# Kernel optimization log

Hardware: AMD Instinct MI355X
Metric: run time of the kernel (lower is better)

Reference implementation:

```python
import jax, jax.numpy as jnp
import numpy as np

N = 50000        # nodes
E = 800000       # directed edges (before self-loops)
NODE_DIM = 128
HIDDEN = 64
HEADS = 4
C = HIDDEN // HEADS   # 16 per-head channels
LAYERS = 4
G = 256          # graphs in batch
EPS = 1e-5       # BatchNorm eps
SLOPE = 0.2      # GAT leaky_relu negative slope


def setup_inputs() -> dict:
    key = jax.random.key(0)
    ks = jax.random.split(key, 12)

    def gl(k, shape, fan_in):  # glorot-ish init
        return jax.random.normal(k, shape, jnp.float32) * np.float32(1.0 / np.sqrt(fan_in))

    x = jax.random.normal(ks[0], (N, NODE_DIM), jnp.float32)
    edge_index = jax.random.randint(ks[1], (2, E), 0, N)
    batch = jnp.sort(jax.random.randint(ks[2], (N,), 0, G))

    return {
        "x": x,
        "embed_W": gl(ks[3], (NODE_DIM, HIDDEN), NODE_DIM),
        "embed_b": jnp.zeros((HIDDEN,), jnp.float32),
        "gat_W": gl(ks[4], (LAYERS, HIDDEN, HIDDEN), HIDDEN),
        "att_src": gl(ks[5], (LAYERS, HEADS, C), C),
        "att_dst": gl(ks[6], (LAYERS, HEADS, C), C),
        "gat_b": jnp.zeros((LAYERS, HIDDEN), jnp.float32),
        "bn_gamma": jnp.ones((LAYERS, HIDDEN), jnp.float32),
        "bn_beta": jnp.zeros((LAYERS, HIDDEN), jnp.float32),
        "fc1_W": gl(ks[7], (HIDDEN, HIDDEN), HIDDEN),
        "fc1_b": jnp.zeros((HIDDEN,), jnp.float32),
        "fc2_W": gl(ks[8], (HIDDEN, 1), HIDDEN),
        "fc2_b": jnp.zeros((1,), jnp.float32),
        "edge_index": edge_index,
        "batch": batch,
    }


def reference(x, embed_W, embed_b, gat_W, att_src, att_dst, gat_b,
              bn_gamma, bn_beta, fc1_W, fc1_b, fc2_W, fc2_b,
              edge_index, batch):
    # GATConv default: add self-loops (message flows src -> dst)
    loops = jnp.arange(N)
    src = jnp.concatenate([edge_index[0], loops])
    dst = jnp.concatenate([edge_index[1], loops])

    h = x @ embed_W + embed_b  # [N, HIDDEN]
    for l in range(LAYERS):
        xp = (h @ gat_W[l]).reshape(N, HEADS, C)          # per-head transform
        a_s = jnp.sum(xp * att_src[l], axis=-1)           # [N, H]
        a_d = jnp.sum(xp * att_dst[l], axis=-1)           # [N, H]
        e = jax.nn.leaky_relu(a_s[src] + a_d[dst], SLOPE) # [E', H]
        # segment softmax over incoming edges of each dst node
        m = jax.ops.segment_max(e, dst, num_segments=N)
        p = jnp.exp(e - m[dst])
        s = jax.ops.segment_sum(p, dst, num_segments=N)
        alpha = p / (s[dst] + 1e-16)                      # [E', H]
        msg = xp[src] * alpha[:, :, None]                 # [E', H, C]
        h = jax.ops.segment_sum(msg, dst, num_segments=N).reshape(N, HIDDEN) + gat_b[l]
        # BatchNorm over nodes (training-mode batch stats, biased variance)
        mu = jnp.mean(h, axis=0)
        var = jnp.var(h, axis=0)
        h = (h - mu) * jax.lax.rsqrt(var + EPS) * bn_gamma[l] + bn_beta[l]
        h = jax.nn.elu(h)

    g = jax.ops.segment_sum(h, batch, num_segments=G)     # global_add_pool
    g = jax.nn.relu(g @ fc1_W + fc1_b)                    # dropout: identity (eval)
    return (g @ fc2_W + fc2_b).reshape(-1)                # [G]
```

## Files before the change

kernel.cpp:

```cpp
#include <hip/hip_runtime.h>

#define N_NODES 50000
#define N_EDGES 800000
#define NODE_DIM 128
#define HIDDEN 64
#define HEADS 4
#define LAYERS 4
#define NGRAPH 256
#define BN_EPS 1e-5f
#define SLOPE 0.2f
#define NTILES 196
#define BN_BLOCKS 256
#define NPW 16
#define GBLK ((N_NODES + 4 * NPW - 1) / (4 * NPW))

typedef unsigned short u16;
typedef unsigned int   u32;

__device__ __forceinline__ float b2f(u16 v) { return __uint_as_float(((u32)v) << 16); }
__device__ __forceinline__ u16 f2b(float f) {
    u32 u = __float_as_uint(f);
    u32 r = (u + 0x7FFFu + ((u >> 16) & 1u)) >> 16;
    return (u16)r;
}
__device__ __forceinline__ float ld(const void* p, int i, int isf) {
    return isf ? ((const float*)p)[i] : b2f(((const u16*)p)[i]);
}

__global__ void k_mark(u16* out, u16 pat) { out[threadIdx.x] = pat; }

__global__ void k_initw(const void* gamma, const void* We, const void* b,
                        const void* gatW, int* flag, int* cnt,
                        float* __restrict__ Wf, float* __restrict__ bf) {
    int isf = (((const u32*)gamma)[0] == 0x3F800000u) ? 1 : 0;
    if (blockIdx.x < NTILES) {
        int i = blockIdx.x * 256 + threadIdx.x;
        if (i < N_NODES) cnt[i] = 0;
        if (i == 0) *flag = isf;
    } else {
        int r = blockIdx.x - NTILES;
        int c = threadIdx.x;
        if (c < HIDDEN) {
            float acc = 0.f;
            if (r < NODE_DIM) {
                for (int k = 0; k < HIDDEN; k++)
                    acc += ld(We, r * HIDDEN + k, isf) * ld(gatW, k * HIDDEN + c, isf);
                Wf[r * HIDDEN + c] = acc;
            } else {
                for (int k = 0; k < HIDDEN; k++)
                    acc += ld(b, k, isf) * ld(gatW, k * HIDDEN + c, isf);
                bf[c] = acc;
            }
        }
    }
}

__global__ void k_count(const int* __restrict__ ei, int* __restrict__ cnt,
                        int* __restrict__ eslot) {
    int e = blockIdx.x * 256 + threadIdx.x;
    if (e >= N_EDGES) return;
    eslot[e] = atomicAdd(&cnt[ei[N_EDGES + e]], 1);
}
__global__ void k_scan1(const int* __restrict__ cnt, int* __restrict__ row_ptr,
                        int* __restrict__ tsum) {
    int b = blockIdx.x, t = threadIdx.x, i = b * 256 + t;
    int c = (i < N_NODES) ? cnt[i] : 0;
    __shared__ int ps[256];
    ps[t] = c;
    __syncthreads();
    for (int off = 1; off < 256; off <<= 1) {
        int v = (t >= off) ? ps[t - off] : 0;
        __syncthreads();
        ps[t] += v;
        __syncthreads();
    }
    if (i < N_NODES) row_ptr[i] = ps[t] - c;
    if (t == 255) tsum[b] = ps[255];
}
__global__ void k_scan3(int* __restrict__ row_ptr, const int* __restrict__ tsum) {
    __shared__ int ps[256];
    int t = threadIdx.x;
    int c = (t < NTILES) ? tsum[t] : 0;
    ps[t] = c;
    __syncthreads();
    for (int off = 1; off < 256; off <<= 1) {
        int v = (t >= off) ? ps[t - off] : 0;
        __syncthreads();
        ps[t] += v;
        __syncthreads();
    }
    int toff_b = (blockIdx.x == 0) ? 0 : ps[blockIdx.x - 1];
    int i = blockIdx.x * 256 + t;
    if (i < N_NODES) row_ptr[i] += toff_b;
    if (i == 0) row_ptr[N_NODES] = N_EDGES;
}
__global__ void k_fill(const int* __restrict__ ei, const int* __restrict__ row_ptr,
                       const int* __restrict__ eslot, int* __restrict__ col) {
    int e = blockIdx.x * 256 + threadIdx.x;
    if (e >= N_EDGES) return;
    col[row_ptr[ei[N_EDGES + e]] + eslot[e]] = ei[e];
}

template<int ISF>
__device__ __forceinline__ float2 ldx2(const void* x, int n, int t) {
    if (ISF) {
        return ((const float2*)x)[(size_t)n * (NODE_DIM / 2) + t];
    } else {
        u32 v = ((const u32*)x)[(size_t)n * (NODE_DIM / 2) + t];
        return make_float2(__uint_as_float(v << 16), __uint_as_float(v & 0xFFFF0000u));
    }
}

template<int ISF>
__device__ __forceinline__ void xform0_body(const void* __restrict__ x,
                                            const float* __restrict__ Wf,
                                            const float* __restrict__ bf,
                                            const void* __restrict__ asrc,
                                            const void* __restrict__ adst,
                                            u16* __restrict__ xp16,
                                            float* __restrict__ a_s,
                                            float* __restrict__ a_d) {
    int w = threadIdx.x >> 6, t = threadIdx.x & 63;
    int n0 = blockIdx.x * (4 * NPW) + w * NPW;
    if (n0 >= N_NODES) return;
    __shared__ float xs[4][2][4][NODE_DIM];
    float wreg[NODE_DIM];
#pragma unroll
    for (int k = 0; k < NODE_DIM; k++) wreg[k] = Wf[k * HIDDEN + t];
    float bias = bf[t];
    float vsc = ld(asrc, t, ISF);
    float vdc = ld(adst, t, ISF);

    float2 r[4], rn[4];
#pragma unroll
    for (int i = 0; i < 4; i++) r[i] = ldx2<ISF>(x, n0 + i, t);
#pragma unroll
    for (int i = 0; i < 4; i++) *(float2*)&xs[w][0][i][2 * t] = r[i];

    for (int g = 0; g < NPW / 4; g++) {
        if (g + 1 < NPW / 4) {
#pragma unroll
            for (int i = 0; i < 4; i++) rn[i] = ldx2<ISF>(x, n0 + (g + 1) * 4 + i, t);
        }
#pragma unroll
        for (int i = 0; i < 4; i++) {
            int n = n0 + g * 4 + i;
            const float* xr = xs[w][g & 1][i];
            float a0 = 0.f, a1 = 0.f, a2 = 0.f, a3 = 0.f;
#pragma unroll
            for (int k = 0; k < NODE_DIM; k += 4) {
                float4 xv = *(const float4*)&xr[k];
                a0 += xv.x * wreg[k];
                a1 += xv.y * wreg[k + 1];
                a2 += xv.z * wreg[k + 2];
                a3 += xv.w * wreg[k + 3];
            }
            float acc = (a0 + a1) + (a2 + a3) + bias;
            xp16[(size_t)n * HIDDEN + t] = f2b(acc);
            float vs = acc * vsc, vd = acc * vdc;
#pragma unroll
            for (int o = 1; o < 16; o <<= 1) {
                vs += __shfl_xor(vs, o, 16);
                vd += __shfl_xor(vd, o, 16);
            }
            if ((t & 15) == 0) {
                a_s[n * HEADS + (t >> 4)] = vs;
                a_d[n * HEADS + (t >> 4)] = vd;
            }
        }
        if (g + 1 < NPW / 4) {
#pragma unroll
            for (int i = 0; i < 4; i++) *(float2*)&xs[w][(g + 1) & 1][i][2 * t] = rn[i];
        }
    }
}
__global__ void __launch_bounds__(256)
k_xform0(const void* __restrict__ x, const float* __restrict__ Wf,
         const float* __restrict__ bf,
         const void* __restrict__ asrc, const void* __restrict__ adst,
         const int* __restrict__ fl,
         u16* __restrict__ xp16, float* __restrict__ a_s, float* __restrict__ a_d,
         float* __restrict__ bn_part) {
    if (blockIdx.x < BN_BLOCKS && threadIdx.x < 128)
        bn_part[blockIdx.x * 128 + threadIdx.x] = 0.f;
    if (*fl) xform0_body<1>(x, Wf, bf, asrc, adst, xp16, a_s, a_d);
    else     xform0_body<0>(x, Wf, bf, asrc, adst, xp16, a_s, a_d);
}

template<int ISF>
__device__ __forceinline__ void transform_body(const float* __restrict__ h,
                                               const void* __restrict__ W,
                                               const void* __restrict__ asrc,
                                               const void* __restrict__ adst, int l,
                                               const float* __restrict__ bnss,
                                               u16* __restrict__ xp16,
                                               float* __restrict__ a_s,
                                               float* __restrict__ a_d) {
    int w = threadIdx.x >> 6, t = threadIdx.x & 63;
    int n0 = blockIdx.x * (4 * NPW) + w * NPW;
    if (n0 >= N_NODES) return;
    __shared__ float hsb[4][2][4][HIDDEN];
    float wreg[HIDDEN];
#pragma unroll
    for (int k = 0; k < HIDDEN; k++) wreg[k] = ld(W, l * HIDDEN * HIDDEN + k * HIDDEN + t, ISF);
    float vsc = ld(asrc, l * HIDDEN + t, ISF);
    float vdc = ld(adst, l * HIDDEN + t, ISF);
    float sc = bnss[t], sh = bnss[64 + t];

    float r[4], rn[4];
#pragma unroll
    for (int i = 0; i < 4; i++) {
        float u = h[(size_t)(n0 + i) * HIDDEN + t];
        u = u * sc + sh;
        r[i] = u > 0.f ? u : (__expf(u) - 1.f);
    }
#pragma unroll
    for (int i = 0; i < 4; i++) hsb[w][0][i][t] = r[i];

    for (int g = 0; g < NPW / 4; g++) {
        if (g + 1 < NPW / 4) {
#pragma unroll
            for (int i = 0; i < 4; i++)
                rn[i] = h[(size_t)(n0 + (g + 1) * 4 + i) * HIDDEN + t];
        }
#pragma unroll
        for (int i = 0; i < 4; i++) {
            int n = n0 + g * 4 + i;
            const float* hr = hsb[w][g & 1][i];
            float c0 = 0.f, c1 = 0.f, c2 = 0.f, c3 = 0.f;
#pragma unroll
            for (int k = 0; k < HIDDEN; k += 4) {
                float4 xv = *(const float4*)&hr[k];
                c0 += xv.x * wreg[k];
                c1 += xv.y * wreg[k + 1];
                c2 += xv.z * wreg[k + 2];
                c3 += xv.w * wreg[k + 3];
            }
            float acc = (c0 + c1) + (c2 + c3);
            xp16[(size_t)n * HIDDEN + t] = f2b(acc);
            float vs = acc * vsc, vd = acc * vdc;
#pragma unroll
            for (int o = 1; o < 16; o <<= 1) {
                vs += __shfl_xor(vs, o, 16);
                vd += __shfl_xor(vd, o, 16);
            }
            if ((t & 15) == 0) {
                a_s[n * HEADS + (t >> 4)] = vs;
                a_d[n * HEADS + (t >> 4)] = vd;
            }
        }
        if (g + 1 < NPW / 4) {
#pragma unroll
            for (int i = 0; i < 4; i++) {
                float u = rn[i] * sc + sh;
                hsb[w][(g + 1) & 1][i][t] = u > 0.f ? u : (__expf(u) - 1.f);
            }
        }
    }
}
__global__ void __launch_bounds__(256)
k_transform(const float* __restrict__ h, const void* __restrict__ W,
            const void* __restrict__ asrc, const void* __restrict__ adst,
            const int* __restrict__ fl, int l,
            const float* __restrict__ bnss,
            u16* __restrict__ xp16, float* __restrict__ a_s,
            float* __restrict__ a_d, float* __restrict__ bn_part) {
    if (blockIdx.x < BN_BLOCKS && threadIdx.x < 128)
        bn_part[blockIdx.x * 128 + threadIdx.x] = 0.f;
    if (*fl) transform_body<1>(h, W, asrc, adst, l, bnss, xp16, a_s, a_d);
    else     transform_body<0>(h, W, asrc, adst, l, bnss, xp16, a_s, a_d);
}

__global__ void __launch_bounds__(256)
k_gather(const int* __restrict__ row_ptr, const int* __restrict__ col,
         const float* __restrict__ a_s, const float* __restrict__ a_d,
         const u16* __restrict__ xp16, float* __restrict__ h,
         float* __restrict__ bn_part) {
    int d = blockIdx.x * 4 + (threadIdx.x >> 6);
    int t = threadIdx.x & 63;
    int hd = t >> 4, l16 = t & 15, hb = hd << 4;
    int beg = row_ptr[d], end = row_ptr[d + 1];
    float ad = a_d[d * HEADS + hd];

    float m = a_s[d * HEADS + hd] + ad;
    m = m > 0.f ? m : SLOPE * m;
    float s = 1.f;
    float acc = b2f(xp16[(size_t)d * HIDDEN + t]);

    for (int j0 = beg; j0 < end; j0 += 16) {
        int jj = j0 + l16;
        int sv = col[jj < end ? jj : end - 1];
        float e = -1e30f;
        if (jj < end) {
            e = a_s[sv * HEADS + hd] + ad;
            e = e > 0.f ? e : SLOPE * e;
        }
        float cm = e;
#pragma unroll
        for (int o = 1; o < 16; o <<= 1) cm = fmaxf(cm, __shfl_xor(cm, o, 16));
        float nm = fmaxf(m, cm);
        float scale = __expf(m - nm);
        float alpha = (jj < end) ? __expf(e - nm) : 0.f;
        float cs = alpha;
#pragma unroll
        for (int o = 1; o < 16; o <<= 1) cs += __shfl_xor(cs, o, 16);
        s = s * scale + cs;
        acc *= scale;
#pragma unroll
        for (int q = 0; q < 16; q++) {
            int   svq = __shfl(sv, q, 64);
            float aq  = __shfl(alpha, hb + q, 64);
            acc += aq * b2f(xp16[(size_t)svq * HIDDEN + t]);
        }
        m = nm;
    }
    float v = acc / (s + 1e-16f);
    h[(size_t)d * HIDDEN + t] = v;

    __shared__ float s1[256];
    __shared__ float s2[256];
    s1[threadIdx.x] = v;
    s2[threadIdx.x] = v * v;
    __syncthreads();
    if (threadIdx.x < 64) {
        float su = s1[t] + s1[64 + t] + s1[128 + t] + s1[192 + t];
        float sq = s2[t] + s2[64 + t] + s2[128 + t] + s2[192 + t];
        float* bp = bn_part + (blockIdx.x & (BN_BLOCKS - 1)) * 128;
        atomicAdd(bp + t, su);
        atomicAdd(bp + 64 + t, sq);
    }
}

__global__ void k_bn_final(const float* __restrict__ bn_part,
                           const void* __restrict__ gamma, const void* __restrict__ beta,
                           const int* __restrict__ fl, int l, float* __restrict__ bnss) {
    int t = threadIdx.x;
    float sum = 0.f, sq = 0.f;
#pragma unroll 8
    for (int b = 0; b < BN_BLOCKS; b++) {
        sum += bn_part[b * 128 + t];
        sq  += bn_part[b * 128 + 64 + t];
    }
    int isf = *fl;
    const float inv_n = 1.f / (float)N_NODES;
    float mu  = sum * inv_n;
    float var = sq * inv_n - mu * mu;
    float sc = rsqrtf(var + BN_EPS) * ld(gamma, l * HIDDEN + t, isf);
    bnss[t]      = sc;
    bnss[64 + t] = ld(beta, l * HIDDEN + t, isf) - mu * sc;
}

__global__ void __launch_bounds__(1024)
k_poolmlp(const float* __restrict__ h, const int* __restrict__ batch,
          const float* __restrict__ bnss,
          const void* __restrict__ W1, const void* __restrict__ b1,
          const void* __restrict__ W2, const void* __restrict__ b2,
          const int* __restrict__ fl, void* __restrict__ out) {
    int gr = blockIdx.x;
    int t = threadIdx.x & 63, w = threadIdx.x >> 6;
    int lo = 0, hi = N_NODES;
    while (lo < hi) { int mid = (lo + hi) >> 1; if (batch[mid] < gr) lo = mid + 1; else hi = mid; }
    int beg = lo;
    lo = 0; hi = N_NODES;
    while (lo < hi) { int mid = (lo + hi) >> 1; if (batch[mid] < gr + 1) lo = mid + 1; else hi = mid; }
    int end = lo;
    float sc = bnss[t], sh = bnss[64 + t];
    float acc = 0.f;
    for (int n = beg + w; n < end; n += 16) {
        float v = h[(size_t)n * HIDDEN + t] * sc + sh;
        acc += v > 0.f ? v : (__expf(v) - 1.f);
    }
    __shared__ float sd[1024];
    __shared__ float gs[64];
    sd[threadIdx.x] = acc;
    __syncthreads();
    if (w < 8) sd[threadIdx.x] += sd[threadIdx.x + 512];
    __syncthreads();
    if (w < 4) sd[threadIdx.x] += sd[threadIdx.x + 256];
    __syncthreads();
    if (w < 2) sd[threadIdx.x] += sd[threadIdx.x + 128];
    __syncthreads();
    if (w == 0) gs[t] = sd[t] + sd[t + 64];
    __syncthreads();
    if (w == 0) {
        int isf = *fl;
        float a1 = ld(b1, t, isf);
        for (int k = 0; k < HIDDEN; k++) a1 += gs[k] * ld(W1, k * HIDDEN + t, isf);
        a1 = fmaxf(a1, 0.f);
        float p = a1 * ld(W2, t, isf);
#pragma unroll
        for (int o = 1; o < 64; o <<= 1) p += __shfl_xor(p, o, 64);
        if (t == 0) {
            float r = p + ld(b2, 0, isf);
            if (isf) ((float*)out)[gr] = r;
            else     ((u16*)out)[gr]   = f2b(r);
        }
    }
}

extern "C" void kernel_launch(void* const* d_in, const int* in_sizes, int n_in,
                              void* d_out, int out_size, void* d_ws, size_t ws_size,
                              hipStream_t stream) {
    u16* out16 = (u16*)d_out;

    bool sizes_ok = (n_in == 15) && (out_size == NGRAPH)
        && in_sizes[0] == N_NODES * NODE_DIM
        && in_sizes[1] == NODE_DIM * HIDDEN
        && in_sizes[2] == HIDDEN
        && in_sizes[3] == LAYERS * HIDDEN * HIDDEN
        && in_sizes[4] == LAYERS * HIDDEN
        && in_sizes[5] == LAYERS * HIDDEN
        && in_sizes[6] == LAYERS * HIDDEN
        && in_sizes[7] == LAYERS * HIDDEN
        && in_sizes[8] == LAYERS * HIDDEN
        && in_sizes[9] == HIDDEN * HIDDEN
        && in_sizes[10] == HIDDEN
        && in_sizes[11] == HIDDEN
        && in_sizes[12] == 1
        && in_sizes[13] == 2 * N_EDGES
        && in_sizes[14] == N_NODES;
    if (!sizes_ok) { k_mark<<<1, 256, 0, stream>>>(out16, 0x4442); return; }

    float* ws      = (float*)d_ws;
    float* h       = ws;
    u16*   xp16    = (u16*)(ws + 3200000);
    float* a_s     = ws + 4800000;
    float* a_d     = ws + 5000000;
    float* bn_part = ws + 5200000;
    float* bnss    = ws + 5232768;
    int* row_ptr   = (int*)(ws + 5232896);
    int* cnt       = row_ptr + 50001;
    int* eslot     = cnt + 50000;
    int* col       = eslot + 800000;
    int* tsum      = col + 800000;
    int* dflag     = tsum + 256;
    float* Wf      = (float*)(dflag + 1);
    float* bf      = Wf + NODE_DIM * HIDDEN;

    const size_t NEED_BYTES =
        (size_t)(5232896 + 50001 + 50000 + 800000 + 800000 + 256 + 1
                 + NODE_DIM * HIDDEN + HIDDEN) * 4;
    if (ws_size < NEED_BYTES) { k_mark<<<1, 256, 0, stream>>>(out16, 0x447A); return; }

    const void* x        = d_in[0];
    const void* embed_W  = d_in[1];
    const void* embed_b  = d_in[2];
    const void* gat_W    = d_in[3];
    const void* att_src  = d_in[4];
    const void* att_dst  = d_in[5];
    const void* bn_gamma = d_in[7];
    const void* bn_beta  = d_in[8];
    const void* fc1_W    = d_in[9];
    const void* fc1_b    = d_in[10];
    const void* fc2_W    = d_in[11];
    const void* fc2_b    = d_in[12];
    const int* ei        = (const int*)d_in[13];
    const int* batch     = (const int*)d_in[14];

    const int e_blocks = (N_EDGES + 255) / 256;
    k_initw<<<NTILES + NODE_DIM + 1, 256, 0, stream>>>(bn_gamma, embed_W, embed_b,
                                                       gat_W, dflag, cnt, Wf, bf);
    k_count<<<e_blocks, 256, 0, stream>>>(ei, cnt, eslot);
    k_scan1<<<NTILES, 256, 0, stream>>>(cnt, row_ptr, tsum);
    k_scan3<<<NTILES, 256, 0, stream>>>(row_ptr, tsum);
    k_fill<<<e_blocks, 256, 0, stream>>>(ei, row_ptr, eslot, col);

    k_xform0<<<GBLK, 256, 0, stream>>>(x, Wf, bf, att_src, att_dst, dflag,
                                       xp16, a_s, a_d, bn_part);

    for (int l = 0; l < LAYERS; l++) {
        if (l > 0)
            k_transform<<<GBLK, 256, 0, stream>>>(h, gat_W, att_src, att_dst,
                                                  dflag, l, bnss,
                                                  xp16, a_s, a_d, bn_part);
        k_gather<<<N_NODES / 4, 256, 0, stream>>>(row_ptr, col, a_s, a_d, xp16, h, bn_part);
        k_bn_final<<<1, 64, 0, stream>>>(bn_part, bn_gamma, bn_beta, dflag, l, bnss);
    }

    k_poolmlp<<<NGRAPH, 1024, 0, stream>>>(h, batch, bnss, fc1_W, fc1_b, fc2_W, fc2_b,
                                           dflag, d_out);
}
```

Measured before the change: 466.8 us.

## Fold BN finalize into consumer kernels and prefetch gather rows

Removes the single-block k_bn_final launch per layer. Each k_transform block and the pool/MLP kernel now reduce the 256 partial BN sums themselves, and the partial buffers are double-buffered so the next layer can zero its own while reading the previous one. The gather kernel also issues all 16 neighbor row loads up front before the softmax shuffles, to raise memory-level parallelism. The trade-off is redundant BN reduction work in every block, about 128 KB of reads per block, plus extra registers in the gather.

Result: no change. 464.7 us (-0.5%).

```diff
diff --git a/kernel.cpp b/kernel.cpp
--- a/kernel.cpp
+++ b/kernel.cpp
@@ -180,9 +180,9 @@
          const void* __restrict__ asrc, const void* __restrict__ adst,
          const int* __restrict__ fl,
          u16* __restrict__ xp16, float* __restrict__ a_s, float* __restrict__ a_d,
-         float* __restrict__ bn_part) {
+         float* __restrict__ bn0) {
     if (blockIdx.x < BN_BLOCKS && threadIdx.x < 128)
-        bn_part[blockIdx.x * 128 + threadIdx.x] = 0.f;
+        bn0[blockIdx.x * 128 + threadIdx.x] = 0.f;
     if (*fl) xform0_body<1>(x, Wf, bf, asrc, adst, xp16, a_s, a_d);
     else     xform0_body<0>(x, Wf, bf, asrc, adst, xp16, a_s, a_d);
 }
@@ -262,20 +262,45 @@
 k_transform(const float* __restrict__ h, const void* __restrict__ W,
             const void* __restrict__ asrc, const void* __restrict__ adst,
             const int* __restrict__ fl, int l,
-            const float* __restrict__ bnss,
+            const float* __restrict__ bn_prev, float* __restrict__ bn_next,
+            const void* __restrict__ gamma, const void* __restrict__ beta,
             u16* __restrict__ xp16, float* __restrict__ a_s,
-            float* __restrict__ a_d, float* __restrict__ bn_part) {
+            float* __restrict__ a_d) {
+    __shared__ float r1[4][64];
+    __shared__ float r2[4][64];
+    __shared__ float bnss_s[128];
+    int t = threadIdx.x & 63, w = threadIdx.x >> 6;
     if (blockIdx.x < BN_BLOCKS && threadIdx.x < 128)
-        bn_part[blockIdx.x * 128 + threadIdx.x] = 0.f;
-    if (*fl) transform_body<1>(h, W, asrc, adst, l, bnss, xp16, a_s, a_d);
-    else     transform_body<0>(h, W, asrc, adst, l, bnss, xp16, a_s, a_d);
+        bn_next[blockIdx.x * 128 + threadIdx.x] = 0.f;
+    float sum = 0.f, sq = 0.f;
+#pragma unroll 8
+    for (int b = w; b < BN_BLOCKS; b += 4) {
+        sum += bn_prev[b * 128 + t];
+        sq  += bn_prev[b * 128 + 64 + t];
+    }
+    r1[w][t] = sum; r2[w][t] = sq;
+    __syncthreads();
+    int isf = *fl;
+    if (threadIdx.x < 64) {
+        float S = r1[0][t] + r1[1][t] + r1[2][t] + r1[3][t];
+        float Q = r2[0][t] + r2[1][t] + r2[2][t] + r2[3][t];
+        const float inv_n = 1.f / (float)N_NODES;
+        float mu  = S * inv_n;
+        float var = Q * inv_n - mu * mu;
+        float sc = rsqrtf(var + BN_EPS) * ld(gamma, l * HIDDEN + t, isf);
+        bnss_s[t]      = sc;
+        bnss_s[64 + t] = ld(beta, l * HIDDEN + t, isf) - mu * sc;
+    }
+    __syncthreads();
+    if (isf) transform_body<1>(h, W, asrc, adst, l, bnss_s, xp16, a_s, a_d);
+    else     transform_body<0>(h, W, asrc, adst, l, bnss_s, xp16, a_s, a_d);
 }
 
 __global__ void __launch_bounds__(256)
 k_gather(const int* __restrict__ row_ptr, const int* __restrict__ col,
          const float* __restrict__ a_s, const float* __restrict__ a_d,
          const u16* __restrict__ xp16, float* __restrict__ h,
-         float* __restrict__ bn_part) {
+         float* __restrict__ bn_out) {
     int d = blockIdx.x * 4 + (threadIdx.x >> 6);
     int t = threadIdx.x & 63;
     int hd = t >> 4, l16 = t & 15, hb = hd << 4;
@@ -290,6 +315,12 @@
     for (int j0 = beg; j0 < end; j0 += 16) {
         int jj = j0 + l16;
         int sv = col[jj < end ? jj : end - 1];
+        int sva[16];
+#pragma unroll
+        for (int q = 0; q < 16; q++) sva[q] = __shfl(sv, q, 64);
+        u16 xv[16];
+#pragma unroll
+        for (int q = 0; q < 16; q++) xv[q] = xp16[(size_t)sva[q] * HIDDEN + t];
         float e = -1e30f;
         if (jj < end) {
             e = a_s[sv * HEADS + hd] + ad;
@@ -307,11 +338,8 @@
         s = s * scale + cs;
         acc *= scale;
 #pragma unroll
-        for (int q = 0; q < 16; q++) {
-            int   svq = __shfl(sv, q, 64);
-            float aq  = __shfl(alpha, hb + q, 64);
-            acc += aq * b2f(xp16[(size_t)svq * HIDDEN + t]);
-        }
+        for (int q = 0; q < 16; q++)
+            acc = fmaf(__shfl(alpha, hb + q, 64), b2f(xv[q]), acc);
         m = nm;
     }
     float v = acc / (s + 1e-16f);
@@ -325,53 +353,61 @@
     if (threadIdx.x < 64) {
         float su = s1[t] + s1[64 + t] + s1[128 + t] + s1[192 + t];
         float sq = s2[t] + s2[64 + t] + s2[128 + t] + s2[192 + t];
-        float* bp = bn_part + (blockIdx.x & (BN_BLOCKS - 1)) * 128;
+        float* bp = bn_out + (blockIdx.x & (BN_BLOCKS - 1)) * 128;
         atomicAdd(bp + t, su);
         atomicAdd(bp + 64 + t, sq);
     }
 }
 
-__global__ void k_bn_final(const float* __restrict__ bn_part,
-                           const void* __restrict__ gamma, const void* __restrict__ beta,
-                           const int* __restrict__ fl, int l, float* __restrict__ bnss) {
-    int t = threadIdx.x;
-    float sum = 0.f, sq = 0.f;
-#pragma unroll 8
-    for (int b = 0; b < BN_BLOCKS; b++) {
-        sum += bn_part[b * 128 + t];
-        sq  += bn_part[b * 128 + 64 + t];
-    }
-    int isf = *fl;
-    const float inv_n = 1.f / (float)N_NODES;
-    float mu  = sum * inv_n;
-    float var = sq * inv_n - mu * mu;
-    float sc = rsqrtf(var + BN_EPS) * ld(gamma, l * HIDDEN + t, isf);
-    bnss[t]      = sc;
-    bnss[64 + t] = ld(beta, l * HIDDEN + t, isf) - mu * sc;
-}
-
 __global__ void __launch_bounds__(1024)
 k_poolmlp(const float* __restrict__ h, const int* __restrict__ batch,
-          const float* __restrict__ bnss,
+          const float* __restrict__ bn_prev,
+          const void* __restrict__ gamma, const void* __restrict__ beta,
           const void* __restrict__ W1, const void* __restrict__ b1,
           const void* __restrict__ W2, const void* __restrict__ b2,
           const int* __restrict__ fl, void* __restrict__ out) {
+    __shared__ float sd[1024];
+    __shared__ float se[1024];
+    __shared__ float gs[64];
+    __shared__ float bnss_s[128];
     int gr = blockIdx.x;
     int t = threadIdx.x & 63, w = threadIdx.x >> 6;
+    int isf = *fl;
+    {
+        float sum = 0.f, sq = 0.f;
+#pragma unroll 4
+        for (int b = w; b < BN_BLOCKS; b += 16) {
+            sum += bn_prev[b * 128 + t];
+            sq  += bn_prev[b * 128 + 64 + t];
+        }
+        sd[threadIdx.x] = sum; se[threadIdx.x] = sq;
+        __syncthreads();
+        if (threadIdx.x < 64) {
+            float S = 0.f, Q = 0.f;
+#pragma unroll
+            for (int j = 0; j < 16; j++) { S += sd[j * 64 + t]; Q += se[j * 64 + t]; }
+            const float inv_n = 1.f / (float)N_NODES;
+            float mu  = S * inv_n;
+            float var = Q * inv_n - mu * mu;
+            float sc = rsqrtf(var + BN_EPS) * ld(gamma, (LAYERS - 1) * HIDDEN + t, isf);
+            bnss_s[t]      = sc;
+            bnss_s[64 + t] = ld(beta, (LAYERS - 1) * HIDDEN + t, isf) - mu * sc;
+        }
+        __syncthreads();
+    }
     int lo = 0, hi = N_NODES;
     while (lo < hi) { int mid = (lo + hi) >> 1; if (batch[mid] < gr) lo = mid + 1; else hi = mid; }
     int beg = lo;
     lo = 0; hi = N_NODES;
     while (lo < hi) { int mid = (lo + hi) >> 1; if (batch[mid] < gr + 1) lo = mid + 1; else hi = mid; }
     int end = lo;
-    float sc = bnss[t], sh = bnss[64 + t];
+    float sc = bnss_s[t], sh = bnss_s[64 + t];
     float acc = 0.f;
     for (int n = beg + w; n < end; n += 16) {
         float v = h[(size_t)n * HIDDEN + t] * sc + sh;
         acc += v > 0.f ? v : (__expf(v) - 1.f);
     }
-    __shared__ float sd[1024];
-    __shared__ float gs[64];
+    __syncthreads();
     sd[threadIdx.x] = acc;
     __syncthreads();
     if (w < 8) sd[threadIdx.x] += sd[threadIdx.x + 512];
@@ -383,7 +419,6 @@
     if (w == 0) gs[t] = sd[t] + sd[t + 64];
     __syncthreads();
     if (w == 0) {
-        int isf = *fl;
         float a1 = ld(b1, t, isf);
         for (int k = 0; k < HIDDEN; k++) a1 += gs[k] * ld(W1, k * HIDDEN + t, isf);
         a1 = fmaxf(a1, 0.f);
@@ -427,8 +462,7 @@
     float* a_s     = ws + 4800000;
     float* a_d     = ws + 5000000;
     float* bn_part = ws + 5200000;
-    float* bnss    = ws + 5232768;
-    int* row_ptr   = (int*)(ws + 5232896);
+    int* row_ptr   = (int*)(ws + 5265536);
     int* cnt       = row_ptr + 50001;
     int* eslot     = cnt + 50000;
     int* col       = eslot + 800000;
@@ -438,7 +472,7 @@
     float* bf      = Wf + NODE_DIM * HIDDEN;
 
     const size_t NEED_BYTES =
-        (size_t)(5232896 + 50001 + 50000 + 800000 + 800000 + 256 + 1
+        (size_t)(5265536 + 50001 + 50000 + 800000 + 800000 + 256 + 1
                  + NODE_DIM * HIDDEN + HIDDEN) * 4;
     if (ws_size < NEED_BYTES) { k_mark<<<1, 256, 0, stream>>>(out16, 0x447A); return; }
 
@@ -457,6 +491,9 @@
     const int* ei        = (const int*)d_in[13];
     const int* batch     = (const int*)d_in[14];
 
+    float* bnA = bn_part;
+    float* bnB = bn_part + 32768;
+
     const int e_blocks = (N_EDGES + 255) / 256;
     k_initw<<<NTILES + NODE_DIM + 1, 256, 0, stream>>>(bn_gamma, embed_W, embed_b,
                                                        gat_W, dflag, cnt, Wf, bf);
@@ -466,17 +503,22 @@
     k_fill<<<e_blocks, 256, 0, stream>>>(ei, row_ptr, eslot, col);
 
     k_xform0<<<GBLK, 256, 0, stream>>>(x, Wf, bf, att_src, att_dst, dflag,
-                                       xp16, a_s, a_d, bn_part);
+                                       xp16, a_s, a_d, bnA);
 
     for (int l = 0; l < LAYERS; l++) {
-        if (l > 0)
+        float* bn_cur = (l & 1) ? bnB : bnA;
+        if (l > 0) {
+            float* bn_prev = ((l - 1) & 1) ? bnB : bnA;
             k_transform<<<GBLK, 256, 0, stream>>>(h, gat_W, att_src, att_dst,
-                                                  dflag, l, bnss,
-                                                  xp16, a_s, a_d, bn_part);
-        k_gather<<<N_NODES / 4, 256, 0, stream>>>(row_ptr, col, a_s, a_d, xp16, h, bn_part);
-        k_bn_final<<<1, 64, 0, stream>>>(bn_part, bn_gamma, bn_beta, dflag, l, bnss);
-    }
-
-    k_poolmlp<<<NGRAPH, 1024, 0, stream>>>(h, batch, bnss, fc1_W, fc1_b, fc2_W, fc2_b,
+                                                  dflag, l, bn_prev, bn_cur,
+                                                  bn_gamma, bn_beta,
+                                                  xp16, a_s, a_d);
+        }
+        k_gather<<<N_NODES / 4, 256, 0, stream>>>(row_ptr, col, a_s, a_d, xp16, h, bn_cur);
+    }
+
+    k_poolmlp<<<NGRAPH, 1024, 0, stream>>>(h, batch, ((LAYERS - 1) & 1) ? bnB : bnA,
+                                           bn_gamma, bn_beta,
+                                           fc1_W, fc1_b, fc2_W, fc2_b,
                                            dflag, d_out);
 }
```
